# Performance work log

Measured on AMD Instinct MI355X. Metric: run time of the kernel, lower is better.

Reference implementation:

```python
import jax, jax.numpy as jnp
import numpy as np

TEMPERATURE = 8.0  # sqrt(d_k), d_k = 64

def setup_inputs() -> dict:
    key = jax.random.key(0)
    kq, kk, kv = jax.random.split(key, 3)
    B, S, D = 16, 4096, 64
    Q = jax.random.normal(kq, (B, S, D), dtype=jnp.float32)
    K = jax.random.normal(kk, (B, S, D), dtype=jnp.float32)
    V = jax.random.normal(kv, (B, S, D), dtype=jnp.float32)
    return {"Q": Q, "K": K, "V": V}

def reference(Q, K, V):
    # scores: [B, S, S]
    scores = jnp.einsum('bqd,bkd->bqk', Q, K) / TEMPERATURE
    attn = jax.nn.softmax(scores, axis=-1)
    # dropout(p=0.1) is identity in eval mode; omitted for deterministic reference
    x = jnp.einsum('bqk,bkd->bqd', attn, V)  # [B, S, D]
    return (x, attn)
```

## Files before the change

kernel.cpp:

```cpp
#include <hip/hip_runtime.h>

#define S 4096
#define D 64
#define NB 16

typedef _Float16 half8 __attribute__((ext_vector_type(8)));
typedef _Float16 half2v __attribute__((ext_vector_type(2)));
typedef float f32x4 __attribute__((ext_vector_type(4)));
typedef int int4v __attribute__((ext_vector_type(4)));

__global__ void cvt_qk(const float* __restrict__ Q, const float* __restrict__ K,
                       _Float16* __restrict__ Qh, _Float16* __restrict__ Kh, int n) {
  int i = blockIdx.x * blockDim.x + threadIdx.x;
  int stride = gridDim.x * blockDim.x;
  for (; i < n; i += stride) {
    Qh[i] = (_Float16)(Q[i] * 0.125f);
    Kh[i] = (_Float16)(K[i]);
  }
}

__global__ void cvt_vt(const float* __restrict__ V, _Float16* __restrict__ Vt) {
  __shared__ float tile[64][65];
  int b = blockIdx.x >> 6;
  int s0 = (blockIdx.x & 63) * 64;
  const float* vb = V + ((size_t)b * S) * D;
  for (int i = threadIdx.x; i < 64 * 64; i += 256) {
    int sl = i >> 6, d = i & 63;
    tile[sl][d] = vb[(size_t)(s0 + sl) * D + d];
  }
  __syncthreads();
  _Float16* vtb = Vt + ((size_t)b * D) * S;
  for (int i = threadIdx.x; i < 64 * 64; i += 256) {
    int dl = i >> 6, sl = i & 63;
    vtb[(size_t)dl * S + s0 + sl] = (_Float16)tile[sl][dl];
  }
}

__global__ __launch_bounds__(512, 4) void attn_lsum(
    const _Float16* __restrict__ Qh, const _Float16* __restrict__ Kh,
    float* __restrict__ Lsum) {
  const int tid = threadIdx.x;
  const int w = tid >> 6;
  const int l = tid & 63;
  const int l15 = l & 15;
  const int lq = l >> 4;
  const int bx = blockIdx.x;
  const int b = bx >> 8;
  const int m0 = (bx & 255) * 16;

  const _Float16* qb = Qh + ((size_t)b * S + m0) * D;
  const _Float16* kb = Kh + ((size_t)b * S) * D;

  __shared__ float lred[8][16];

  half8 qf0 = *(const half8*)(qb + (size_t)l15 * D + lq * 8);
  half8 qf1 = *(const half8*)(qb + (size_t)l15 * D + 32 + lq * 8);

  const int nbase = w * 512;
  const _Float16* kp0 = kb + (size_t)(nbase + l15) * D + lq * 8;

  half8 kc0 = *(const half8*)(kp0);
  half8 kc1 = *(const half8*)(kp0 + 32);
  half8 kn0 = *(const half8*)(kp0 + (size_t)16 * D);
  half8 kn1 = *(const half8*)(kp0 + (size_t)16 * D + 32);

  float vsum = 0.f;
#pragma unroll 1
  for (int s = 0; s < 32; ++s) {
    half8 km0 = kc0, km1 = kc1;
    if (s < 30) {
      const _Float16* kp = kp0 + (size_t)((s + 2) * 16) * D;
      km0 = *(const half8*)(kp);
      km1 = *(const half8*)(kp + 32);
    }
    f32x4 a = (f32x4){0.f, 0.f, 0.f, 0.f};
    a = __builtin_amdgcn_mfma_f32_16x16x32_f16(kc0, qf0, a, 0, 0, 0);
    a = __builtin_amdgcn_mfma_f32_16x16x32_f16(kc1, qf1, a, 0, 0, 0);
    vsum += (__expf(a[0]) + __expf(a[1])) + (__expf(a[2]) + __expf(a[3]));
    kc0 = kn0; kc1 = kn1;
    kn0 = km0; kn1 = km1;
  }

  vsum += __shfl_xor(vsum, 16, 64);
  vsum += __shfl_xor(vsum, 32, 64);
  if (l < 16) lred[w][l] = vsum;
  __syncthreads();
  if (tid < 16) {
    float s = 0.f;
#pragma unroll
    for (int ww = 0; ww < 8; ++ww) s += lred[ww][tid];
    Lsum[(size_t)b * S + m0 + tid] = __logf(s);
  }
}

__global__ __launch_bounds__(512, 2) void attn_main(
    const _Float16* __restrict__ Qh, const _Float16* __restrict__ Kh,
    const _Float16* __restrict__ Vt, const float* __restrict__ Lsum,
    float* __restrict__ X, float* __restrict__ Aout) {
  const int tid = threadIdx.x;
  const int w = tid >> 6;
  const int l = tid & 63;
  const int l15 = l & 15;
  const int lq = l >> 4;
  const int r4 = lq * 4;
  const int bx = blockIdx.x;
  const int b = bx >> 8;
  const int m0 = (bx & 255) * 16;

  const _Float16* qb = Qh + ((size_t)b * S + m0) * D;
  const _Float16* kb = Kh + ((size_t)b * S) * D;
  const _Float16* vtb = Vt + ((size_t)b * D) * S;

  __shared__ __align__(16) float xred[8][16][66];

  half8 qf0 = *(const half8*)(qb + (size_t)l15 * D + lq * 8);
  half8 qf1 = *(const half8*)(qb + (size_t)l15 * D + 32 + lq * 8);

  const float ls = Lsum[(size_t)b * S + m0 + l15];
  const int nbase = w * 512;
  const int srcA = (lq & 1) * 32 + l15;
  const int srcB = srcA + 16;
  const bool hi = (lq & 2) != 0;

  const _Float16* kp0 = kb + (size_t)(nbase + l15) * D + lq * 8;
  const _Float16* vp0 = vtb + (size_t)l15 * S + nbase + lq * 8;
  float* arow = Aout + ((size_t)(b * S + m0 + l15)) * S + nbase + r4;

  f32x4 xacc[4];
#pragma unroll
  for (int fd = 0; fd < 4; ++fd) xacc[fd] = (f32x4){0.f, 0.f, 0.f, 0.f};

  half8 kc0 = *(const half8*)(kp0);
  half8 kc1 = *(const half8*)(kp0 + 32);

#pragma unroll 1
  for (int s = 0; s < 16; ++s) {
    const _Float16* vs = vp0 + s * 32;
    half8 bf0 = *(const half8*)(vs);
    half8 bf1 = *(const half8*)(vs + 16 * S);
    half8 bf2 = *(const half8*)(vs + 32 * S);
    half8 bf3 = *(const half8*)(vs + 48 * S);
    const _Float16* k1p = kp0 + (size_t)(s * 32 + 16) * D;
    half8 k10 = *(const half8*)(k1p);
    half8 k11 = *(const half8*)(k1p + 32);
    half8 kn0 = kc0, kn1 = kc1;
    if (s < 15) {
      const _Float16* knp = kp0 + (size_t)((s + 1) * 32) * D;
      kn0 = *(const half8*)(knp);
      kn1 = *(const half8*)(knp + 32);
    }
    f32x4 a0 = (f32x4){0.f, 0.f, 0.f, 0.f};
    a0 = __builtin_amdgcn_mfma_f32_16x16x32_f16(kc0, qf0, a0, 0, 0, 0);
    a0 = __builtin_amdgcn_mfma_f32_16x16x32_f16(kc1, qf1, a0, 0, 0, 0);
    f32x4 o0;
#pragma unroll
    for (int j = 0; j < 4; ++j) o0[j] = __expf(a0[j] - ls);
    *(f32x4*)(arow + s * 32) = o0;
    half2v h01 = {(_Float16)o0[0], (_Float16)o0[1]};
    half2v h23 = {(_Float16)o0[2], (_Float16)o0[3]};
    int dw0x = __builtin_bit_cast(int, h01);
    int dw0y = __builtin_bit_cast(int, h23);
    f32x4 a1 = (f32x4){0.f, 0.f, 0.f, 0.f};
    a1 = __builtin_amdgcn_mfma_f32_16x16x32_f16(k10, qf0, a1, 0, 0, 0);
    a1 = __builtin_amdgcn_mfma_f32_16x16x32_f16(k11, qf1, a1, 0, 0, 0);
    f32x4 o1;
#pragma unroll
    for (int j = 0; j < 4; ++j) o1[j] = __expf(a1[j] - ls);
    *(f32x4*)(arow + s * 32 + 16) = o1;
    half2v g01 = {(_Float16)o1[0], (_Float16)o1[1]};
    half2v g23 = {(_Float16)o1[2], (_Float16)o1[3]};
    int dw1x = __builtin_bit_cast(int, g01);
    int dw1y = __builtin_bit_cast(int, g23);
    int yA0 = __shfl(dw0x, srcA, 64), yA1 = __shfl(dw0y, srcA, 64);
    int yB0 = __shfl(dw0x, srcB, 64), yB1 = __shfl(dw0y, srcB, 64);
    int xA0 = __shfl(dw1x, srcA, 64), xA1 = __shfl(dw1y, srcA, 64);
    int xB0 = __shfl(dw1x, srcB, 64), xB1 = __shfl(dw1y, srcB, 64);
    int4v ai = {hi ? xA0 : yA0, hi ? xA1 : yA1, hi ? xB0 : yB0, hi ? xB1 : yB1};
    half8 af = __builtin_bit_cast(half8, ai);
    xacc[0] = __builtin_amdgcn_mfma_f32_16x16x32_f16(af, bf0, xacc[0], 0, 0, 0);
    xacc[1] = __builtin_amdgcn_mfma_f32_16x16x32_f16(af, bf1, xacc[1], 0, 0, 0);
    xacc[2] = __builtin_amdgcn_mfma_f32_16x16x32_f16(af, bf2, xacc[2], 0, 0, 0);
    xacc[3] = __builtin_amdgcn_mfma_f32_16x16x32_f16(af, bf3, xacc[3], 0, 0, 0);
    kc0 = kn0;
    kc1 = kn1;
  }

#pragma unroll
  for (int fd = 0; fd < 4; ++fd)
#pragma unroll
    for (int j = 0; j < 4; ++j)
      xred[w][r4 + j][fd * 16 + l15] = xacc[fd][j];
  __syncthreads();
  float* xrow = X + ((size_t)b * S + m0) * D;
#pragma unroll
  for (int o = tid; o < 16 * 64; o += 512) {
    int r = o >> 6, d = o & 63;
    float s = 0.f;
#pragma unroll
    for (int ww = 0; ww < 8; ++ww) s += xred[ww][r][d];
    xrow[(size_t)r * D + d] = s;
  }
}

extern "C" void kernel_launch(void* const* d_in, const int* in_sizes, int n_in,
                              void* d_out, int out_size, void* d_ws, size_t ws_size,
                              hipStream_t stream) {
  const float* Q = (const float*)d_in[0];
  const float* K = (const float*)d_in[1];
  const float* V = (const float*)d_in[2];
  float* X = (float*)d_out;
  float* A = X + (size_t)NB * S * D;
  _Float16* Qh = (_Float16*)d_ws;
  _Float16* Kh = Qh + (size_t)NB * S * D;
  _Float16* Vt = Kh + (size_t)NB * S * D;
  float* Lsum = (float*)(Vt + (size_t)NB * S * D);
  int n = NB * S * D;
  cvt_qk<<<2048, 256, 0, stream>>>(Q, K, Qh, Kh, n);
  cvt_vt<<<NB * 64, 256, 0, stream>>>(V, Vt);
  attn_lsum<<<NB * 256, 512, 0, stream>>>(Qh, Kh, Lsum);
  attn_main<<<NB * 256, 512, 0, stream>>>(Qh, Kh, Vt, Lsum, X, A);
}
```

Measured before the change: 828.4 us.

## Fuse softmax normalizer and attention into one kernel with per-wave query tiles

Replaces the separate row-sum kernel and the main attention kernel with a single kernel. Each wave now owns a whole 16-row query tile. It first sweeps all keys to compute the log-sum-exp, then sweeps again to write the attention probabilities and accumulate the output. This removes a kernel launch, the Lsum round trip through global memory, and the LDS cross-wave reduction with its barrier. In exchange, each wave runs a much longer serial loop, and the grid shrinks to 512 blocks, so there is less parallel slack to hide latency.

```diff
diff --git a/kernel.cpp b/kernel.cpp
--- a/kernel.cpp
+++ b/kernel.cpp
@@ -36,105 +36,71 @@
   }
 }
 
-__global__ __launch_bounds__(512, 4) void attn_lsum(
+__global__ __launch_bounds__(512, 2) void attn_all(
     const _Float16* __restrict__ Qh, const _Float16* __restrict__ Kh,
-    float* __restrict__ Lsum) {
-  const int tid = threadIdx.x;
-  const int w = tid >> 6;
-  const int l = tid & 63;
-  const int l15 = l & 15;
-  const int lq = l >> 4;
-  const int bx = blockIdx.x;
-  const int b = bx >> 8;
-  const int m0 = (bx & 255) * 16;
-
-  const _Float16* qb = Qh + ((size_t)b * S + m0) * D;
-  const _Float16* kb = Kh + ((size_t)b * S) * D;
-
-  __shared__ float lred[8][16];
-
-  half8 qf0 = *(const half8*)(qb + (size_t)l15 * D + lq * 8);
-  half8 qf1 = *(const half8*)(qb + (size_t)l15 * D + 32 + lq * 8);
-
-  const int nbase = w * 512;
-  const _Float16* kp0 = kb + (size_t)(nbase + l15) * D + lq * 8;
-
-  half8 kc0 = *(const half8*)(kp0);
-  half8 kc1 = *(const half8*)(kp0 + 32);
-  half8 kn0 = *(const half8*)(kp0 + (size_t)16 * D);
-  half8 kn1 = *(const half8*)(kp0 + (size_t)16 * D + 32);
-
-  float vsum = 0.f;
-#pragma unroll 1
-  for (int s = 0; s < 32; ++s) {
-    half8 km0 = kc0, km1 = kc1;
-    if (s < 30) {
-      const _Float16* kp = kp0 + (size_t)((s + 2) * 16) * D;
-      km0 = *(const half8*)(kp);
-      km1 = *(const half8*)(kp + 32);
-    }
-    f32x4 a = (f32x4){0.f, 0.f, 0.f, 0.f};
-    a = __builtin_amdgcn_mfma_f32_16x16x32_f16(kc0, qf0, a, 0, 0, 0);
-    a = __builtin_amdgcn_mfma_f32_16x16x32_f16(kc1, qf1, a, 0, 0, 0);
-    vsum += (__expf(a[0]) + __expf(a[1])) + (__expf(a[2]) + __expf(a[3]));
-    kc0 = kn0; kc1 = kn1;
-    kn0 = km0; kn1 = km1;
-  }
-
-  vsum += __shfl_xor(vsum, 16, 64);
-  vsum += __shfl_xor(vsum, 32, 64);
-  if (l < 16) lred[w][l] = vsum;
-  __syncthreads();
-  if (tid < 16) {
-    float s = 0.f;
-#pragma unroll
-    for (int ww = 0; ww < 8; ++ww) s += lred[ww][tid];
-    Lsum[(size_t)b * S + m0 + tid] = __logf(s);
-  }
-}
-
-__global__ __launch_bounds__(512, 2) void attn_main(
-    const _Float16* __restrict__ Qh, const _Float16* __restrict__ Kh,
-    const _Float16* __restrict__ Vt, const float* __restrict__ Lsum,
-    float* __restrict__ X, float* __restrict__ Aout) {
+    const _Float16* __restrict__ Vt, float* __restrict__ X,
+    float* __restrict__ Aout) {
   const int tid = threadIdx.x;
   const int w = tid >> 6;
   const int l = tid & 63;
   const int l15 = l & 15;
   const int lq = l >> 4;
   const int r4 = lq * 4;
-  const int bx = blockIdx.x;
-  const int b = bx >> 8;
-  const int m0 = (bx & 255) * 16;
+  const int qt = blockIdx.x * 8 + w;
+  const int b = qt >> 8;
+  const int m0 = (qt & 255) * 16;
 
   const _Float16* qb = Qh + ((size_t)b * S + m0) * D;
   const _Float16* kb = Kh + ((size_t)b * S) * D;
   const _Float16* vtb = Vt + ((size_t)b * D) * S;
 
-  __shared__ __align__(16) float xred[8][16][66];
-
   half8 qf0 = *(const half8*)(qb + (size_t)l15 * D + lq * 8);
   half8 qf1 = *(const half8*)(qb + (size_t)l15 * D + 32 + lq * 8);
 
-  const float ls = Lsum[(size_t)b * S + m0 + l15];
-  const int nbase = w * 512;
   const int srcA = (lq & 1) * 32 + l15;
   const int srcB = srcA + 16;
   const bool hi = (lq & 2) != 0;
 
-  const _Float16* kp0 = kb + (size_t)(nbase + l15) * D + lq * 8;
-  const _Float16* vp0 = vtb + (size_t)l15 * S + nbase + lq * 8;
-  float* arow = Aout + ((size_t)(b * S + m0 + l15)) * S + nbase + r4;
+  const _Float16* kp0 = kb + (size_t)l15 * D + lq * 8;
+  const _Float16* vp0 = vtb + (size_t)l15 * S + lq * 8;
+
+  float vsum = 0.f;
+  half8 kc0 = *(const half8*)(kp0);
+  half8 kc1 = *(const half8*)(kp0 + 32);
+#pragma unroll 1
+  for (int s = 0; s < 128; ++s) {
+    const _Float16* k1p = kp0 + (size_t)(s * 32 + 16) * D;
+    half8 k10 = *(const half8*)(k1p);
+    half8 k11 = *(const half8*)(k1p + 32);
+    half8 kn0 = kc0, kn1 = kc1;
+    if (s < 127) {
+      const _Float16* knp = kp0 + (size_t)((s + 1) * 32) * D;
+      kn0 = *(const half8*)(knp);
+      kn1 = *(const half8*)(knp + 32);
+    }
+    f32x4 a0 = (f32x4){0.f, 0.f, 0.f, 0.f};
+    a0 = __builtin_amdgcn_mfma_f32_16x16x32_f16(kc0, qf0, a0, 0, 0, 0);
+    a0 = __builtin_amdgcn_mfma_f32_16x16x32_f16(kc1, qf1, a0, 0, 0, 0);
+    vsum += (__expf(a0[0]) + __expf(a0[1])) + (__expf(a0[2]) + __expf(a0[3]));
+    f32x4 a1 = (f32x4){0.f, 0.f, 0.f, 0.f};
+    a1 = __builtin_amdgcn_mfma_f32_16x16x32_f16(k10, qf0, a1, 0, 0, 0);
+    a1 = __builtin_amdgcn_mfma_f32_16x16x32_f16(k11, qf1, a1, 0, 0, 0);
+    vsum += (__expf(a1[0]) + __expf(a1[1])) + (__expf(a1[2]) + __expf(a1[3]));
+    kc0 = kn0; kc1 = kn1;
+  }
+  vsum += __shfl_xor(vsum, 16, 64);
+  vsum += __shfl_xor(vsum, 32, 64);
+  const float ls = __logf(vsum);
 
   f32x4 xacc[4];
 #pragma unroll
   for (int fd = 0; fd < 4; ++fd) xacc[fd] = (f32x4){0.f, 0.f, 0.f, 0.f};
+  float* arow = Aout + ((size_t)(b * S + m0 + l15)) * S + r4;
 
-  half8 kc0 = *(const half8*)(kp0);
-  half8 kc1 = *(const half8*)(kp0 + 32);
-
+  kc0 = *(const half8*)(kp0);
+  kc1 = *(const half8*)(kp0 + 32);
 #pragma unroll 1
-  for (int s = 0; s < 16; ++s) {
+  for (int s = 0; s < 128; ++s) {
     const _Float16* vs = vp0 + s * 32;
     half8 bf0 = *(const half8*)(vs);
     half8 bf1 = *(const half8*)(vs + 16 * S);
@@ -144,7 +110,7 @@
     half8 k10 = *(const half8*)(k1p);
     half8 k11 = *(const half8*)(k1p + 32);
     half8 kn0 = kc0, kn1 = kc1;
-    if (s < 15) {
+    if (s < 127) {
       const _Float16* knp = kp0 + (size_t)((s + 1) * 32) * D;
       kn0 = *(const half8*)(knp);
       kn1 = *(const half8*)(knp + 32);
@@ -181,25 +147,15 @@
     xacc[1] = __builtin_amdgcn_mfma_f32_16x16x32_f16(af, bf1, xacc[1], 0, 0, 0);
     xacc[2] = __builtin_amdgcn_mfma_f32_16x16x32_f16(af, bf2, xacc[2], 0, 0, 0);
     xacc[3] = __builtin_amdgcn_mfma_f32_16x16x32_f16(af, bf3, xacc[3], 0, 0, 0);
-    kc0 = kn0;
-    kc1 = kn1;
+    kc0 = kn0; kc1 = kn1;
   }
 
+  float* xb = X + ((size_t)b * S + m0) * D;
 #pragma unroll
   for (int fd = 0; fd < 4; ++fd)
 #pragma unroll
     for (int j = 0; j < 4; ++j)
-      xred[w][r4 + j][fd * 16 + l15] = xacc[fd][j];
-  __syncthreads();
-  float* xrow = X + ((size_t)b * S + m0) * D;
-#pragma unroll
-  for (int o = tid; o < 16 * 64; o += 512) {
-    int r = o >> 6, d = o & 63;
-    float s = 0.f;
-#pragma unroll
-    for (int ww = 0; ww < 8; ++ww) s += xred[ww][r][d];
-    xrow[(size_t)r * D + d] = s;
-  }
+      xb[(size_t)(r4 + j) * D + fd * 16 + l15] = xacc[fd][j];
 }
 
 extern "C" void kernel_launch(void* const* d_in, const int* in_sizes, int n_in,
@@ -213,10 +169,8 @@
   _Float16* Qh = (_Float16*)d_ws;
   _Float16* Kh = Qh + (size_t)NB * S * D;
   _Float16* Vt = Kh + (size_t)NB * S * D;
-  float* Lsum = (float*)(Vt + (size_t)NB * S * D);
   int n = NB * S * D;
   cvt_qk<<<2048, 256, 0, stream>>>(Q, K, Qh, Kh, n);
   cvt_vt<<<NB * 64, 256, 0, stream>>>(V, Vt);
-  attn_lsum<<<NB * 256, 512, 0, stream>>>(Qh, Kh, Lsum);
-  attn_main<<<NB * 256, 512, 0, stream>>>(Qh, Kh, Vt, Lsum, X, A);
+  attn_all<<<512, 512, 0, stream>>>(Qh, Kh, Vt, X, A);
 }
```

Result: no change. 832.6 us (+0.5%).
